# Optimization experiments

Measured on AMD Instinct MI355X. Metric: run time of the kernel, lower is better.

## Reference

```python
import jax, jax.numpy as jnp
import numpy as np

IMG_W, IMG_H = 1024, 800  # normalization constants baked into the module


def setup_inputs() -> dict:
    key = jax.random.key(0)
    kf, kx, kw_, ky, kh = jax.random.split(key, 5)
    B, C, H, W, N = 2, 512, 50, 64, 128
    features = jax.random.normal(kf, (B, C, H, W), dtype=jnp.float32)
    # Valid boxes in pixel coords: x2 > x1, y2 > y1, inside the 1024x800 image
    x1 = jax.random.uniform(kx, (B, N), dtype=jnp.float32) * 940.0
    bw = 20.0 + jax.random.uniform(kw_, (B, N), dtype=jnp.float32) * 64.0
    y1 = jax.random.uniform(ky, (B, N), dtype=jnp.float32) * 720.0
    bh = 20.0 + jax.random.uniform(kh, (B, N), dtype=jnp.float32) * 64.0
    roiss = jnp.stack([x1, y1, x1 + bw, y1 + bh], axis=-1)  # [B, N, 4]
    return {"features": features, "roiss": roiss}


def reference(features, roiss):
    # features: [B, C, H, W]; roiss: [B, N, 4] (x1, y1, x2, y2) pixel coords
    B, C, H, W = features.shape
    norm = roiss / jnp.array([IMG_W, IMG_H, IMG_W, IMG_H], dtype=roiss.dtype)
    x1 = jnp.clip(jnp.floor(norm[..., 0] * W).astype(jnp.int32), 0)  # [B, N]
    y1 = jnp.clip(jnp.floor(norm[..., 1] * H).astype(jnp.int32), 0)
    x2 = jnp.clip(jnp.ceil(norm[..., 2] * W).astype(jnp.int32), 0)
    y2 = jnp.clip(jnp.ceil(norm[..., 3] * H).astype(jnp.int32), 0)
    # Degenerate-box fixes from the original per-ROI loop
    x2 = jnp.where((x1 == 0) & (x2 == 0), x2 + 1, x2)
    y2 = jnp.where((y1 == 0) & (y2 == 0), y2 + 1, y2)
    x1 = jnp.where(x1 >= W, W - 1, x1)
    y1 = jnp.where(y1 >= H, H - 1, y1)
    # Region membership masks (half-open slices feat[:, y1:y2, x1:x2])
    hs = jnp.arange(H)
    ws = jnp.arange(W)
    row = (hs[None, None, :] >= y1[..., None]) & (hs[None, None, :] < y2[..., None])  # [B,N,H]
    col = (ws[None, None, :] >= x1[..., None]) & (ws[None, None, :] < x2[..., None])  # [B,N,W]
    mask = row[:, :, :, None] & col[:, :, None, :]  # [B, N, H, W]
    neg = jnp.asarray(-jnp.inf, features.dtype)
    # AdaptiveMaxPool2d((1,1)) over each cropped region == masked global max
    masked = jnp.where(mask[:, :, None, :, :], features[:, None, :, :, :], neg)  # [B,N,C,H,W]
    pooled = masked.max(axis=(-2, -1))  # [B, N, C]
    # Original returns a per-image list of [N, C * 1 * 1]; stacked here as [B, N, C]
    return pooled
```

## Files before the change

kernel.cpp:

```cpp
#include <hip/hip_runtime.h>
#include <hip/hip_bf16.h>
#include <math.h>

#define IMG_W_F 1024.0f
#define IMG_H_F 800.0f

__global__ __launch_bounds__(256) void roipool_kernel(
    const float* __restrict__ feat,
    const float* __restrict__ rois,
    float* __restrict__ out,
    int B, int C, int H, int W, int N)
{
    const int bn = blockIdx.x;
    const int b  = bn / N;

    const float* roi = rois + (size_t)bn * 4;
    const float rx1 = roi[0], ry1 = roi[1], rx2 = roi[2], ry2 = roi[3];

    int x1 = (int)floorf(rx1 / IMG_W_F * (float)W);
    int y1 = (int)floorf(ry1 / IMG_H_F * (float)H);
    int x2 = (int)ceilf (rx2 / IMG_W_F * (float)W);
    int y2 = (int)ceilf (ry2 / IMG_H_F * (float)H);
    x1 = max(x1, 0);
    y1 = max(y1, 0);
    x2 = max(x2, 0);
    y2 = max(y2, 0);

    if (x1 == 0 && x2 == 0) x2 = 1;
    if (y1 == 0 && y2 == 0) y2 = 1;
    if (x1 >= W) x1 = W - 1;
    if (y1 >= H) y1 = H - 1;

    const int ye = min(y2, H);
    const int xe = min(x2, W);

    const float* fb = feat + (size_t)b * C * H * W;
    float* ob = out + (size_t)bn * C;

    for (int c = threadIdx.x; c < C; c += blockDim.x) {
        const float* fc = fb + (size_t)c * H * W;
        float m = -INFINITY;
        for (int y = y1; y < ye; ++y) {
            const float* fr = fc + (size_t)y * W;
            for (int x = x1; x < xe; ++x) {
                m = fmaxf(m, fr[x]);
            }
        }
        ob[c] = m;
    }
}

extern "C" void kernel_launch(void* const* d_in, const int* in_sizes, int n_in,
                              void* d_out, int out_size, void* d_ws, size_t ws_size,
                              hipStream_t stream) {
    const int B = 2, C = 512, H = 50, W = 64, N = 128;

    const float* feat = (const float*)d_in[0];
    const float* rois = (const float*)d_in[1];
    float* out = (float*)d_out;

    dim3 grid(B * N);
    dim3 block(256);
    roipool_kernel<<<grid, block, 0, stream>>>(feat, rois, out, B, C, H, W, N);
}
```

Before: 75.15 us.

## Transpose features to channel-last before ROI max pooling for coalesced reads

Adds a tiled shared-memory transpose that converts the feature map from CHW to HWC in the workspace, then runs a new pooling kernel with 512 threads per ROI. Adjacent threads read adjacent channels, so each feature access is coalesced instead of each thread walking its own strided channel plane. It costs an extra pass over the 13 MB feature tensor and a second launch, and it falls back to the old direct kernel when the workspace is too small.

Measured after the change: 76.25 us. About the same (+1.5%).

```diff
diff --git a/kernel.cpp b/kernel.cpp
--- a/kernel.cpp
+++ b/kernel.cpp
@@ -5,7 +5,76 @@
 #define IMG_W_F 1024.0f
 #define IMG_H_F 800.0f
 
-__global__ __launch_bounds__(256) void roipool_kernel(
+__global__ __launch_bounds__(256) void transpose_chw_to_hwc(
+    const float* __restrict__ in,
+    float* __restrict__ out,
+    int C, int HW)
+{
+    __shared__ float tile[32][33];
+    const int b   = blockIdx.z;
+    const int hw0 = blockIdx.x * 32;
+    const int c0  = blockIdx.y * 32;
+    const int tx  = threadIdx.x;
+    const int ty  = threadIdx.y;
+
+    const float* ib = in  + (size_t)b * C * HW;
+    float*       ob = out + (size_t)b * C * HW;
+
+#pragma unroll
+    for (int i = 0; i < 4; ++i) {
+        const int r = ty + i * 8;
+        tile[r][tx] = ib[(size_t)(c0 + r) * HW + (hw0 + tx)];
+    }
+    __syncthreads();
+#pragma unroll
+    for (int i = 0; i < 4; ++i) {
+        const int r = ty + i * 8;
+        ob[(size_t)(hw0 + r) * C + (c0 + tx)] = tile[tx][r];
+    }
+}
+
+__global__ __launch_bounds__(512) void roipool_cl_kernel(
+    const float* __restrict__ ft,
+    const float* __restrict__ rois,
+    float* __restrict__ out,
+    int C, int H, int W, int N)
+{
+    const int bn = blockIdx.x;
+    const int b  = bn / N;
+
+    const float* roi = rois + (size_t)bn * 4;
+    const float rx1 = roi[0], ry1 = roi[1], rx2 = roi[2], ry2 = roi[3];
+
+    int x1 = (int)floorf(rx1 / IMG_W_F * (float)W);
+    int y1 = (int)floorf(ry1 / IMG_H_F * (float)H);
+    int x2 = (int)ceilf (rx2 / IMG_W_F * (float)W);
+    int y2 = (int)ceilf (ry2 / IMG_H_F * (float)H);
+    x1 = max(x1, 0);
+    y1 = max(y1, 0);
+    x2 = max(x2, 0);
+    y2 = max(y2, 0);
+    if (x1 == 0 && x2 == 0) x2 = 1;
+    if (y1 == 0 && y2 == 0) y2 = 1;
+    if (x1 >= W) x1 = W - 1;
+    if (y1 >= H) y1 = H - 1;
+    const int ye = min(y2, H);
+    const int xe = min(x2, W);
+
+    const float* fb = ft + (size_t)b * H * W * C;
+
+    for (int c = threadIdx.x; c < C; c += blockDim.x) {
+        float m = -INFINITY;
+        for (int y = y1; y < ye; ++y) {
+            const float* fr = fb + ((size_t)y * W) * C + c;
+            for (int x = x1; x < xe; ++x) {
+                m = fmaxf(m, fr[(size_t)x * C]);
+            }
+        }
+        out[(size_t)bn * C + c] = m;
+    }
+}
+
+__global__ __launch_bounds__(256) void roipool_direct_kernel(
     const float* __restrict__ feat,
     const float* __restrict__ rois,
     float* __restrict__ out,
@@ -21,16 +90,11 @@
     int y1 = (int)floorf(ry1 / IMG_H_F * (float)H);
     int x2 = (int)ceilf (rx2 / IMG_W_F * (float)W);
     int y2 = (int)ceilf (ry2 / IMG_H_F * (float)H);
-    x1 = max(x1, 0);
-    y1 = max(y1, 0);
-    x2 = max(x2, 0);
-    y2 = max(y2, 0);
-
+    x1 = max(x1, 0); y1 = max(y1, 0); x2 = max(x2, 0); y2 = max(y2, 0);
     if (x1 == 0 && x2 == 0) x2 = 1;
     if (y1 == 0 && y2 == 0) y2 = 1;
     if (x1 >= W) x1 = W - 1;
     if (y1 >= H) y1 = H - 1;
-
     const int ye = min(y2, H);
     const int xe = min(x2, W);
 
@@ -42,9 +106,7 @@
         float m = -INFINITY;
         for (int y = y1; y < ye; ++y) {
             const float* fr = fc + (size_t)y * W;
-            for (int x = x1; x < xe; ++x) {
-                m = fmaxf(m, fr[x]);
-            }
+            for (int x = x1; x < xe; ++x) m = fmaxf(m, fr[x]);
         }
         ob[c] = m;
     }
@@ -54,12 +116,27 @@
                               void* d_out, int out_size, void* d_ws, size_t ws_size,
                               hipStream_t stream) {
     const int B = 2, C = 512, H = 50, W = 64, N = 128;
+    const int HW = H * W;
 
     const float* feat = (const float*)d_in[0];
     const float* rois = (const float*)d_in[1];
     float* out = (float*)d_out;
 
-    dim3 grid(B * N);
-    dim3 block(256);
-    roipool_kernel<<<grid, block, 0, stream>>>(feat, rois, out, B, C, H, W, N);
+    const size_t need = (size_t)B * C * HW * sizeof(float);
+
+    if (ws_size >= need) {
+        float* feat_t = (float*)d_ws;
+
+        dim3 tgrid(HW / 32, C / 32, B);
+        dim3 tblock(32, 8);
+        transpose_chw_to_hwc<<<tgrid, tblock, 0, stream>>>(feat, feat_t, C, HW);
+
+        dim3 pgrid(B * N);
+        dim3 pblock(512);
+        roipool_cl_kernel<<<pgrid, pblock, 0, stream>>>(feat_t, rois, out, C, H, W, N);
+    } else {
+        dim3 grid(B * N);
+        dim3 block(256);
+        roipool_direct_kernel<<<grid, block, 0, stream>>>(feat, rois, out, B, C, H, W, N);
+    }
 }
```

## Spread ROI window across wave lanes and split channels over grid

Applied to the files above, without the earlier changes.

Each 64-lane wave now handles 32 channels. Its lanes cover an 8x8 tiling of the ROI window, and a shuffle-xor reduction across the wave combines the partial maxima. The grid gains a second dimension over channel groups of 128, so there are four times as many blocks. Before, each thread scanned a whole window for one channel, which gave strided, uncoalesced loads and long serial loops. The new layout puts neighbouring lanes on neighbouring x positions, at the cost of six shuffles per channel, and assumes C is a multiple of 128.

After: 80.39 us. +7.0%, slower.

```diff
diff --git a/kernel.cpp b/kernel.cpp
--- a/kernel.cpp
+++ b/kernel.cpp
@@ -5,11 +5,11 @@
 #define IMG_W_F 1024.0f
 #define IMG_H_F 800.0f
 
-__global__ __launch_bounds__(256) void roipool_kernel(
+__global__ __launch_bounds__(256) void roipool_fused(
     const float* __restrict__ feat,
     const float* __restrict__ rois,
     float* __restrict__ out,
-    int B, int C, int H, int W, int N)
+    int C, int H, int W, int N)
 {
     const int bn = blockIdx.x;
     const int b  = bn / N;
@@ -25,28 +25,45 @@
     y1 = max(y1, 0);
     x2 = max(x2, 0);
     y2 = max(y2, 0);
-
     if (x1 == 0 && x2 == 0) x2 = 1;
     if (y1 == 0 && y2 == 0) y2 = 1;
     if (x1 >= W) x1 = W - 1;
     if (y1 >= H) y1 = H - 1;
-
     const int ye = min(y2, H);
     const int xe = min(x2, W);
 
+    const int lane = threadIdx.x & 63;
+    const int wv   = threadIdx.x >> 6;
+    const int c0   = blockIdx.y * 128 + wv * 32;
+    const int dy   = lane >> 3;
+    const int dx   = lane & 7;
+
     const float* fb = feat + (size_t)b * C * H * W;
-    float* ob = out + (size_t)bn * C;
 
-    for (int c = threadIdx.x; c < C; c += blockDim.x) {
-        const float* fc = fb + (size_t)c * H * W;
+    float res = 0.0f;
+#pragma unroll 8
+    for (int i = 0; i < 32; ++i) {
+        const int c = c0 + i;
+        const float* fc = fb + (size_t)c * (H * W);
+
         float m = -INFINITY;
-        for (int y = y1; y < ye; ++y) {
-            const float* fr = fc + (size_t)y * W;
-            for (int x = x1; x < xe; ++x) {
-                m = fmaxf(m, fr[x]);
+        for (int ty = y1 + dy; ty < ye; ty += 8) {
+            const float* fr = fc + ty * W;
+            for (int tx = x1 + dx; tx < xe; tx += 8) {
+                m = fmaxf(m, fr[tx]);
             }
         }
-        ob[c] = m;
+
+#pragma unroll
+        for (int off = 32; off > 0; off >>= 1) {
+            m = fmaxf(m, __shfl_xor(m, off, 64));
+        }
+
+        if (lane == i) res = m;
+    }
+
+    if (lane < 32) {
+        out[(size_t)bn * C + c0 + lane] = res;
     }
 }
 
@@ -59,7 +76,7 @@
     const float* rois = (const float*)d_in[1];
     float* out = (float*)d_out;
 
-    dim3 grid(B * N);
+    dim3 grid(B * N, C / 128);
     dim3 block(256);
-    roipool_kernel<<<grid, block, 0, stream>>>(feat, rois, out, B, C, H, W, N);
+    roipool_fused<<<grid, block, 0, stream>>>(feat, rois, out, C, H, W, N);
 }
```
